# Performance work log

Hardware: AMD Instinct MI355X
Metric: run time of the kernel (lower is better)

Reference implementation:

```python
import jax, jax.numpy as jnp
import numpy as np
from math import sqrt

B, H, S, D = 4, 16, 2048, 64
NEG = -1000000000.0

def setup_inputs() -> dict:
    key = jax.random.key(0)
    kq, kk, kv, km = jax.random.split(key, 4)
    Q = jax.random.normal(kq, (B, H, S, D), dtype=jnp.float32)
    K = jax.random.normal(kk, (B, H, S, D), dtype=jnp.float32)
    V = jax.random.normal(kv, (B, H, S, D), dtype=jnp.float32)
    mask = jax.random.uniform(km, (B, 1, S, S)) < 0.1
    return {"Q": Q, "K": K, "V": V, "mask": mask}

def reference(Q, K, V, mask) -> jnp.ndarray:
    # scores: [B,H,S,S]
    scores = jnp.einsum('bhqd,bhkd->bhqk', Q, K)
    scores = jnp.where(mask, NEG, scores)
    attn = jax.nn.softmax(scores / sqrt(Q.shape[-1]), axis=-1)
    return jnp.einsum('bhqk,bhkd->bhqd', attn, V)
```

## Files before the change

kernel.cpp:

```cpp
#include <hip/hip_runtime.h>


#define SEQ 2048
#define DIM 64
#define NBH 64
#define LOG2E 1.44269504088896340736f
#define SCL (0.125f * LOG2E)
#define NEG_SCALED -1.25e8f

typedef short bf16x8 __attribute__((ext_vector_type(8)));
typedef float f32x4 __attribute__((ext_vector_type(4)));

static __device__ __forceinline__ unsigned short f2bf(float f) {
    unsigned int u = __float_as_uint(f);
    u += 0x7fffu + ((u >> 16) & 1u);
    return (unsigned short)(u >> 16);
}

#define GLD16(gp, lp) __builtin_amdgcn_global_load_lds( \
    (const __attribute__((address_space(1))) unsigned int*)(gp), \
    (__attribute__((address_space(3))) unsigned int*)(lp), 16, 0, 0)

__global__ __launch_bounds__(256)
void cvt_k_kernel(const float* __restrict__ K, unsigned short* __restrict__ Kb) {
    size_t i0 = ((size_t)blockIdx.x * 256 + threadIdx.x) * 8;
    float4 a = *(const float4*)(K + i0);
    float4 b = *(const float4*)(K + i0 + 4);
    union { uint4 u; unsigned short s[8]; } w;
    w.s[0] = f2bf(a.x); w.s[1] = f2bf(a.y); w.s[2] = f2bf(a.z); w.s[3] = f2bf(a.w);
    w.s[4] = f2bf(b.x); w.s[5] = f2bf(b.y); w.s[6] = f2bf(b.z); w.s[7] = f2bf(b.w);
    *(uint4*)(Kb + i0) = w.u;
}

__global__ __launch_bounds__(256)
void cvt_vt_kernel(const float* __restrict__ V, unsigned short* __restrict__ Vt) {
    __shared__ __align__(16) unsigned short T[64 * 64];
    const int bh = blockIdx.y;
    const int k0 = blockIdx.x * 64;
    const int t  = threadIdx.x;

    {
        const int kk = t >> 2;
        const int c  = t & 3;
        const int cs = c ^ ((kk >> 3) & 3);
        const float* vp = V + ((size_t)bh * SEQ + k0 + kk) * DIM + c * 16;
        union { uint4 u[2]; unsigned short s[16]; } w;
        #pragma unroll
        for (int j = 0; j < 16; ++j) w.s[j] = f2bf(vp[j]);
        *(uint4*)&T[kk * 64 + cs * 16]     = w.u[0];
        *(uint4*)&T[kk * 64 + cs * 16 + 8] = w.u[1];
    }
    __syncthreads();

    {
        const int kc = t & 7;
        const int dp = t >> 3;
        const int ch = (dp >> 3) ^ (kc & 3);
        const unsigned int* T32 = (const unsigned int*)T;
        union { uint4 u; unsigned short s[8]; } o0, o1;
        #pragma unroll
        for (int i = 0; i < 8; ++i) {
            unsigned int v = T32[(8 * kc + i) * 32 + ch * 8 + (dp & 7)];
            o0.s[i] = (unsigned short)v;
            o1.s[i] = (unsigned short)(v >> 16);
        }
        unsigned short* op = Vt + ((size_t)bh * DIM + 2 * dp) * SEQ + k0 + 8 * kc;
        *(uint4*)op         = o0.u;
        *(uint4*)(op + SEQ) = o1.u;
    }
}

__global__ __launch_bounds__(256)
void pack_mask_kernel(const int* __restrict__ M, unsigned int* __restrict__ Mp) {
    size_t w = (size_t)blockIdx.x * 256 + threadIdx.x;
    const int4* p = (const int4*)(M + w * 32);
    unsigned int m = 0;
    #pragma unroll
    for (int j = 0; j < 8; ++j) {
        int4 v = p[j];
        m |= (unsigned int)(v.x != 0) << (4 * j);
        m |= (unsigned int)(v.y != 0) << (4 * j + 1);
        m |= (unsigned int)(v.z != 0) << (4 * j + 2);
        m |= (unsigned int)(v.w != 0) << (4 * j + 3);
    }
    Mp[w] = m;
}

__global__ __launch_bounds__(256, 4)
void attn_main_kernel(const float* __restrict__ Q,
                      const unsigned short* __restrict__ Kb,
                      const unsigned short* __restrict__ Vt,
                      const unsigned int* __restrict__ Mp,
                      float* __restrict__ O)
{
    const int bh   = blockIdx.y;
    const int b    = bh >> 4;
    const int q0   = blockIdx.x * 128;
    const int tid  = threadIdx.x;
    const int wave = tid >> 6;
    const int lane = tid & 63;
    const int quad = lane >> 4;
    const int l16  = lane & 15;

    __shared__ __align__(16) unsigned short Kt[2][32 * 64];
    __shared__ __align__(16) unsigned short Vs[2][64 * 32];
    __shared__ __align__(16) unsigned short P[4][32][36];

    const unsigned short* Kbh = Kb + (size_t)bh * SEQ * DIM;
    const unsigned short* Vbh = Vt + (size_t)bh * SEQ * DIM;

    bf16x8 qf[2][2];
    {
        const float* Qb = Q + (size_t)bh * SEQ * DIM;
        #pragma unroll
        for (int qh = 0; qh < 2; ++qh) {
            const float* qp = Qb + (size_t)(q0 + wave * 32 + qh * 16 + l16) * DIM + quad * 8;
            #pragma unroll
            for (int dc = 0; dc < 2; ++dc) {
                float4 x = *(const float4*)(qp + dc * 32);
                float4 y = *(const float4*)(qp + dc * 32 + 4);
                qf[qh][dc][0] = (short)f2bf(x.x * SCL); qf[qh][dc][1] = (short)f2bf(x.y * SCL);
                qf[qh][dc][2] = (short)f2bf(x.z * SCL); qf[qh][dc][3] = (short)f2bf(x.w * SCL);
                qf[qh][dc][4] = (short)f2bf(y.x * SCL); qf[qh][dc][5] = (short)f2bf(y.y * SCL);
                qf[qh][dc][6] = (short)f2bf(y.z * SCL); qf[qh][dc][7] = (short)f2bf(y.w * SCL);
            }
        }
    }

    const int kkey  = wave * 8 + (lane >> 3);
    const int kclog = (lane & 7) ^ (lane >> 3);
    const unsigned short* kg = Kbh + (size_t)kkey * DIM + kclog * 8;
    const int vd    = wave * 16 + (lane >> 2);
    const int vclog = (lane & 3) ^ ((lane >> 2) & 3);
    const unsigned short* vg = Vbh + (size_t)vd * SEQ + vclog * 8;
    unsigned short* kl[2] = { &Kt[0][wave * 512], &Kt[1][wave * 512] };
    unsigned short* vl[2] = { &Vs[0][wave * 512], &Vs[1][wave * 512] };

    const unsigned int* mrow = Mp + ((size_t)b * SEQ + q0 + wave * 32) * (SEQ / 32);

    f32x4 acc[2][4];
    #pragma unroll
    for (int qh = 0; qh < 2; ++qh)
        #pragma unroll
        for (int dg = 0; dg < 4; ++dg) acc[qh][dg] = (f32x4){0.f, 0.f, 0.f, 0.f};
    float lsum[2][4] = {{0.f,0.f,0.f,0.f},{0.f,0.f,0.f,0.f}};

    GLD16(kg, kl[0]);
    GLD16(vg, vl[0]);

    for (int it = 0; it < SEQ / 32; ++it) {
        __syncthreads();

        unsigned int mw[2][4];
        #pragma unroll
        for (int qh = 0; qh < 2; ++qh)
            #pragma unroll
            for (int r = 0; r < 4; ++r)
                mw[qh][r] = mrow[(qh * 16 + quad * 4 + r) * (SEQ / 32) + it];

        if (it + 1 < SEQ / 32) {
            const unsigned short* kgn = kg + (size_t)(it + 1) * 32 * DIM;
            const unsigned short* vgn = vg + (size_t)(it + 1) * 32;
            int nb = (it + 1) & 1;
            GLD16(kgn, kl[nb]);
            GLD16(vgn, vl[nb]);
        }

        const unsigned short* Ktb = Kt[it & 1];
        const unsigned short* Vsb = Vs[it & 1];

        f32x4 sc[2][2];
        sc[0][0] = (f32x4){0.f,0.f,0.f,0.f}; sc[0][1] = (f32x4){0.f,0.f,0.f,0.f};
        sc[1][0] = (f32x4){0.f,0.f,0.f,0.f}; sc[1][1] = (f32x4){0.f,0.f,0.f,0.f};
        #pragma unroll
        for (int nt = 0; nt < 2; ++nt) {
            #pragma unroll
            for (int dc = 0; dc < 2; ++dc) {
                const int key = nt * 16 + l16;
                const int cst = (dc * 4 + quad) ^ (l16 & 7);
                bf16x8 kf = *(const bf16x8*)(Ktb + key * DIM + cst * 8);
                sc[0][nt] = __builtin_amdgcn_mfma_f32_16x16x32_bf16(qf[0][dc], kf, sc[0][nt], 0, 0, 0);
                sc[1][nt] = __builtin_amdgcn_mfma_f32_16x16x32_bf16(qf[1][dc], kf, sc[1][nt], 0, 0, 0);
            }
        }

        #pragma unroll
        for (int qh = 0; qh < 2; ++qh) {
            #pragma unroll
            for (int r = 0; r < 4; ++r) {
                unsigned int t = mw[qh][r] >> l16;
                float a0 = __builtin_amdgcn_exp2f(sc[qh][0][r]);
                float a1 = __builtin_amdgcn_exp2f(sc[qh][1][r]);
                a0 = (t & 1u) ? 0.f : a0;
                a1 = (t & 0x10000u) ? 0.f : a1;
                lsum[qh][r] += a0 + a1;
                unsigned int u0 = __float_as_uint(a0) + 0x8000u;
                unsigned int u1 = __float_as_uint(a1) + 0x8000u;
                unsigned int pk = __builtin_amdgcn_perm(u1, u0, 0x07060302u);
                const int row = qh * 16 + quad * 4 + r;
                P[wave][row][l16]      = (unsigned short)pk;
                P[wave][row][l16 + 16] = (unsigned short)(pk >> 16);
            }
        }

        bf16x8 pf0 = *(const bf16x8*)&P[wave][l16][quad * 8];
        bf16x8 pf1 = *(const bf16x8*)&P[wave][16 + l16][quad * 8];

        #pragma unroll
        for (int dg = 0; dg < 4; ++dg) {
            const int d   = dg * 16 + l16;
            const int cst = quad ^ (l16 & 3);
            bf16x8 vf = *(const bf16x8*)(Vsb + d * 32 + cst * 8);
            acc[0][dg] = __builtin_amdgcn_mfma_f32_16x16x32_bf16(pf0, vf, acc[0][dg], 0, 0, 0);
            acc[1][dg] = __builtin_amdgcn_mfma_f32_16x16x32_bf16(pf1, vf, acc[1][dg], 0, 0, 0);
        }
    }

    float* Ob = O + (size_t)bh * SEQ * DIM;
    #pragma unroll
    for (int qh = 0; qh < 2; ++qh) {
        #pragma unroll
        for (int r = 0; r < 4; ++r) {
            float l = lsum[qh][r];
            #pragma unroll
            for (int off = 1; off < 16; off <<= 1)
                l += __shfl_xor(l, off, 16);
            float inv = 1.f / l;
            const int row = q0 + wave * 32 + qh * 16 + quad * 4 + r;
            #pragma unroll
            for (int dg = 0; dg < 4; ++dg)
                Ob[(size_t)row * DIM + dg * 16 + l16] = acc[qh][dg][r] * inv;
        }
    }
}

__global__ __launch_bounds__(256)
void attn_fallback_kernel(const float* __restrict__ Q,
                          const float* __restrict__ K,
                          const float* __restrict__ V,
                          const int* __restrict__ mask,
                          float* __restrict__ O)
{
    const int bh   = blockIdx.y;
    const int b    = bh >> 4;
    const int q0   = blockIdx.x * 64;
    const int tid  = threadIdx.x;
    const int wave = tid >> 6;
    const int lane = tid & 63;
    const int quad = lane >> 4;
    const int l16  = lane & 15;

    __shared__ __align__(16) unsigned short Klds[32][72];
    __shared__ __align__(16) unsigned short VT[64][40];
    __shared__ __align__(16) unsigned short Plds[4][16][40];

    const float* Qb = Q + (size_t)bh * SEQ * DIM;
    const float* Kb = K + (size_t)bh * SEQ * DIM;
    const float* Vb = V + (size_t)bh * SEQ * DIM;
    const int*   Mb = mask + (size_t)b * SEQ * SEQ;

    const int qrow_frag = q0 + wave * 16 + l16;
    bf16x8 qf0, qf1;
    {
        const float* qp = Qb + (size_t)qrow_frag * DIM + quad * 8;
        #pragma unroll
        for (int i = 0; i < 8; ++i) {
            qf0[i] = (short)f2bf(qp[i]);
            qf1[i] = (short)f2bf(qp[32 + i]);
        }
    }

    f32x4 acc[4];
    #pragma unroll
    for (int dg = 0; dg < 4; ++dg) acc[dg] = (f32x4){0.f, 0.f, 0.f, 0.f};
    float mrowv[4] = {-INFINITY, -INFINITY, -INFINITY, -INFINITY};
    float lrow[4] = {0.f, 0.f, 0.f, 0.f};

    const int skey = tid >> 3;
    const int sd0  = (tid & 7) * 8;
    const int vkey = tid & 31;
    const int vd0  = (tid >> 5) * 8;
    const int qrow_m = q0 + wave * 16 + quad * 4;

    for (int kb = 0; kb < SEQ; kb += 32) {
        __syncthreads();
        {
            const float* kp = Kb + (size_t)(kb + skey) * DIM + sd0;
            union { uint4 u4; unsigned short s[8]; } kw;
            #pragma unroll
            for (int i = 0; i < 8; ++i) kw.s[i] = f2bf(kp[i]);
            *(uint4*)&Klds[skey][sd0] = kw.u4;
        }
        {
            const float* vp = Vb + (size_t)(kb + vkey) * DIM + vd0;
            #pragma unroll
            for (int i = 0; i < 8; ++i) VT[vd0 + i][vkey] = f2bf(vp[i]);
        }
        __syncthreads();

        f32x4 sc[2];
        sc[0] = (f32x4){0.f, 0.f, 0.f, 0.f};
        sc[1] = (f32x4){0.f, 0.f, 0.f, 0.f};
        #pragma unroll
        for (int nt = 0; nt < 2; ++nt) {
            bf16x8 kf0 = *(const bf16x8*)&Klds[nt * 16 + l16][quad * 8];
            bf16x8 kf1 = *(const bf16x8*)&Klds[nt * 16 + l16][32 + quad * 8];
            sc[nt] = __builtin_amdgcn_mfma_f32_16x16x32_bf16(qf0, kf0, sc[nt], 0, 0, 0);
            sc[nt] = __builtin_amdgcn_mfma_f32_16x16x32_bf16(qf1, kf1, sc[nt], 0, 0, 0);
        }

        float x[2][4];
        #pragma unroll
        for (int nt = 0; nt < 2; ++nt)
            #pragma unroll
            for (int r = 0; r < 4; ++r) {
                int mv = Mb[(size_t)(qrow_m + r) * SEQ + kb + nt * 16 + l16];
                x[nt][r] = mv ? NEG_SCALED : sc[nt][r] * 0.125f;
            }

        float p[2][4];
        #pragma unroll
        for (int r = 0; r < 4; ++r) {
            float rm = fmaxf(x[0][r], x[1][r]);
            #pragma unroll
            for (int off = 1; off < 16; off <<= 1)
                rm = fmaxf(rm, __shfl_xor(rm, off, 16));
            float mn = fmaxf(mrowv[r], rm);
            float alpha = exp2f((mrowv[r] - mn) * LOG2E);
            mrowv[r] = mn;
            float p0 = exp2f((x[0][r] - mn) * LOG2E);
            float p1 = exp2f((x[1][r] - mn) * LOG2E);
            p[0][r] = p0; p[1][r] = p1;
            float rs = p0 + p1;
            #pragma unroll
            for (int off = 1; off < 16; off <<= 1)
                rs += __shfl_xor(rs, off, 16);
            lrow[r] = lrow[r] * alpha + rs;
            #pragma unroll
            for (int dg = 0; dg < 4; ++dg)
                acc[dg][r] *= alpha;
        }

        #pragma unroll
        for (int nt = 0; nt < 2; ++nt)
            #pragma unroll
            for (int r = 0; r < 4; ++r)
                Plds[wave][quad * 4 + r][nt * 16 + l16] = f2bf(p[nt][r]);

        bf16x8 pf = *(const bf16x8*)&Plds[wave][l16][quad * 8];

        #pragma unroll
        for (int dg = 0; dg < 4; ++dg) {
            bf16x8 vf = *(const bf16x8*)&VT[dg * 16 + l16][quad * 8];
            acc[dg] = __builtin_amdgcn_mfma_f32_16x16x32_bf16(pf, vf, acc[dg], 0, 0, 0);
        }
    }

    float* Ob = O + (size_t)bh * SEQ * DIM;
    #pragma unroll
    for (int r = 0; r < 4; ++r) {
        float inv = 1.f / lrow[r];
        #pragma unroll
        for (int dg = 0; dg < 4; ++dg)
            Ob[(size_t)(qrow_m + r) * DIM + dg * 16 + l16] = acc[dg][r] * inv;
    }
}

extern "C" void kernel_launch(void* const* d_in, const int* in_sizes, int n_in,
                              void* d_out, int out_size, void* d_ws, size_t ws_size,
                              hipStream_t stream) {
    const float* Q = (const float*)d_in[0];
    const float* K = (const float*)d_in[1];
    const float* V = (const float*)d_in[2];
    const int* mask = (const int*)d_in[3];
    float*        O = (float*)d_out;

    const size_t szK = (size_t)NBH * SEQ * DIM * 2;
    const size_t szV = (size_t)NBH * SEQ * DIM * 2;
    const size_t szM = (size_t)4 * SEQ * (SEQ / 32) * 4;
    const size_t need = szK + szV + szM;

    if (ws_size >= need) {
        unsigned short* Kb = (unsigned short*)d_ws;
        unsigned short* Vt = (unsigned short*)((char*)d_ws + szK);
        unsigned int*   Mp = (unsigned int*)((char*)d_ws + szK + szV);

        cvt_k_kernel<<<dim3((NBH * SEQ * DIM) / (256 * 8)), 256, 0, stream>>>(K, Kb);
        cvt_vt_kernel<<<dim3(SEQ / 64, NBH), 256, 0, stream>>>(V, Vt);
        pack_mask_kernel<<<dim3((4 * SEQ * (SEQ / 32)) / 256), 256, 0, stream>>>(mask, Mp);
        attn_main_kernel<<<dim3(SEQ / 128, NBH), 256, 0, stream>>>(Q, Kb, Vt, Mp, O);
    } else {
        attn_fallback_kernel<<<dim3(SEQ / 64, NBH), 256, 0, stream>>>(Q, K, V, mask, O);
    }
}
```

Before: 302.7 us.

## Switch attention to 32x32 MFMA with register-only P exchange and fused prep kernel

Rewrites the main attention loop around 32x32x16 bf16 MFMA. S is computed as K·Q^T, so each lane owns one query row and the probabilities pass to the PV MFMA through a cross-half lane shuffle rather than a shared-memory round trip. The mask is packed in a transposed layout so each lane loads a single word per iteration. The three preprocessing kernels are merged into one launch to cut launch overhead. In exchange it raises register pressure with 16-wide accumulators and adds a loop unroll.

```diff
diff --git a/kernel.cpp b/kernel.cpp
--- a/kernel.cpp
+++ b/kernel.cpp
@@ -10,6 +10,7 @@
 
 typedef short bf16x8 __attribute__((ext_vector_type(8)));
 typedef float f32x4 __attribute__((ext_vector_type(4)));
+typedef float f32x16 __attribute__((ext_vector_type(16)));
 
 static __device__ __forceinline__ unsigned short f2bf(float f) {
     unsigned int u = __float_as_uint(f);
@@ -22,75 +23,78 @@
     (__attribute__((address_space(3))) unsigned int*)(lp), 16, 0, 0)
 
 __global__ __launch_bounds__(256)
-void cvt_k_kernel(const float* __restrict__ K, unsigned short* __restrict__ Kb) {
-    size_t i0 = ((size_t)blockIdx.x * 256 + threadIdx.x) * 8;
-    float4 a = *(const float4*)(K + i0);
-    float4 b = *(const float4*)(K + i0 + 4);
-    union { uint4 u; unsigned short s[8]; } w;
-    w.s[0] = f2bf(a.x); w.s[1] = f2bf(a.y); w.s[2] = f2bf(a.z); w.s[3] = f2bf(a.w);
-    w.s[4] = f2bf(b.x); w.s[5] = f2bf(b.y); w.s[6] = f2bf(b.z); w.s[7] = f2bf(b.w);
-    *(uint4*)(Kb + i0) = w.u;
-}
-
-__global__ __launch_bounds__(256)
-void cvt_vt_kernel(const float* __restrict__ V, unsigned short* __restrict__ Vt) {
-    __shared__ __align__(16) unsigned short T[64 * 64];
-    const int bh = blockIdx.y;
-    const int k0 = blockIdx.x * 64;
-    const int t  = threadIdx.x;
-
-    {
-        const int kk = t >> 2;
-        const int c  = t & 3;
-        const int cs = c ^ ((kk >> 3) & 3);
-        const float* vp = V + ((size_t)bh * SEQ + k0 + kk) * DIM + c * 16;
-        union { uint4 u[2]; unsigned short s[16]; } w;
-        #pragma unroll
-        for (int j = 0; j < 16; ++j) w.s[j] = f2bf(vp[j]);
-        *(uint4*)&T[kk * 64 + cs * 16]     = w.u[0];
-        *(uint4*)&T[kk * 64 + cs * 16 + 8] = w.u[1];
-    }
-    __syncthreads();
-
-    {
-        const int kc = t & 7;
-        const int dp = t >> 3;
-        const int ch = (dp >> 3) ^ (kc & 3);
-        const unsigned int* T32 = (const unsigned int*)T;
-        union { uint4 u; unsigned short s[8]; } o0, o1;
-        #pragma unroll
-        for (int i = 0; i < 8; ++i) {
-            unsigned int v = T32[(8 * kc + i) * 32 + ch * 8 + (dp & 7)];
-            o0.s[i] = (unsigned short)v;
-            o1.s[i] = (unsigned short)(v >> 16);
-        }
-        unsigned short* op = Vt + ((size_t)bh * DIM + 2 * dp) * SEQ + k0 + 8 * kc;
-        *(uint4*)op         = o0.u;
-        *(uint4*)(op + SEQ) = o1.u;
-    }
-}
-
-__global__ __launch_bounds__(256)
-void pack_mask_kernel(const int* __restrict__ M, unsigned int* __restrict__ Mp) {
-    size_t w = (size_t)blockIdx.x * 256 + threadIdx.x;
-    const int4* p = (const int4*)(M + w * 32);
-    unsigned int m = 0;
-    #pragma unroll
-    for (int j = 0; j < 8; ++j) {
-        int4 v = p[j];
-        m |= (unsigned int)(v.x != 0) << (4 * j);
-        m |= (unsigned int)(v.y != 0) << (4 * j + 1);
-        m |= (unsigned int)(v.z != 0) << (4 * j + 2);
-        m |= (unsigned int)(v.w != 0) << (4 * j + 3);
-    }
-    Mp[w] = m;
+void prep_all_kernel(const float* __restrict__ K, const float* __restrict__ V,
+                     const int* __restrict__ M,
+                     unsigned short* __restrict__ Kb, unsigned short* __restrict__ Vt,
+                     unsigned int* __restrict__ Mpt) {
+    const int x = blockIdx.x;
+    const int t = threadIdx.x;
+    if (x < 4096) {
+        size_t i0 = ((size_t)x * 256 + t) * 8;
+        float4 a = *(const float4*)(K + i0);
+        float4 b = *(const float4*)(K + i0 + 4);
+        union { uint4 u; unsigned short s[8]; } w;
+        w.s[0] = f2bf(a.x); w.s[1] = f2bf(a.y); w.s[2] = f2bf(a.z); w.s[3] = f2bf(a.w);
+        w.s[4] = f2bf(b.x); w.s[5] = f2bf(b.y); w.s[6] = f2bf(b.z); w.s[7] = f2bf(b.w);
+        *(uint4*)(Kb + i0) = w.u;
+    } else if (x < 6144) {
+        __shared__ __align__(16) unsigned short T[64 * 64];
+        const int vb = x - 4096;
+        const int bh = vb >> 5;
+        const int k0 = (vb & 31) * 64;
+        {
+            const int kk = t >> 2;
+            const int c  = t & 3;
+            const int cs = c ^ ((kk >> 3) & 3);
+            const float* vp = V + ((size_t)bh * SEQ + k0 + kk) * DIM + c * 16;
+            union { uint4 u[2]; unsigned short s[16]; } w;
+            #pragma unroll
+            for (int j = 0; j < 16; ++j) w.s[j] = f2bf(vp[j]);
+            *(uint4*)&T[kk * 64 + cs * 16]     = w.u[0];
+            *(uint4*)&T[kk * 64 + cs * 16 + 8] = w.u[1];
+        }
+        __syncthreads();
+        {
+            const int kc = t & 7;
+            const int dp = t >> 3;
+            const int ch = (dp >> 3) ^ (kc & 3);
+            const unsigned int* T32 = (const unsigned int*)T;
+            union { uint4 u; unsigned short s[8]; } o0, o1;
+            #pragma unroll
+            for (int i = 0; i < 8; ++i) {
+                unsigned int v = T32[(8 * kc + i) * 32 + ch * 8 + (dp & 7)];
+                o0.s[i] = (unsigned short)v;
+                o1.s[i] = (unsigned short)(v >> 16);
+            }
+            unsigned short* op = Vt + ((size_t)bh * DIM + 2 * dp) * SEQ + k0 + 8 * kc;
+            *(uint4*)op         = o0.u;
+            *(uint4*)(op + SEQ) = o1.u;
+        }
+    } else {
+        const int g = (x - 6144) * 256 + t;
+        const int b = g >> 17;
+        const int r = g & 131071;
+        const int q = r >> 6;
+        const int it = r & 63;
+        const int4* p = (const int4*)(M + (((size_t)b * SEQ + q) * SEQ + it * 32));
+        unsigned int m = 0;
+        #pragma unroll
+        for (int j = 0; j < 8; ++j) {
+            int4 v = p[j];
+            m |= (unsigned int)(v.x != 0) << (4 * j);
+            m |= (unsigned int)(v.y != 0) << (4 * j + 1);
+            m |= (unsigned int)(v.z != 0) << (4 * j + 2);
+            m |= (unsigned int)(v.w != 0) << (4 * j + 3);
+        }
+        Mpt[((size_t)b * 64 + it) * SEQ + q] = m;
+    }
 }
 
 __global__ __launch_bounds__(256, 4)
 void attn_main_kernel(const float* __restrict__ Q,
                       const unsigned short* __restrict__ Kb,
                       const unsigned short* __restrict__ Vt,
-                      const unsigned int* __restrict__ Mp,
+                      const unsigned int* __restrict__ Mpt,
                       float* __restrict__ O)
 {
     const int bh   = blockIdx.y;
@@ -99,31 +103,26 @@
     const int tid  = threadIdx.x;
     const int wave = tid >> 6;
     const int lane = tid & 63;
-    const int quad = lane >> 4;
-    const int l16  = lane & 15;
+    const int h    = lane >> 5;
+    const int q32  = lane & 31;
 
     __shared__ __align__(16) unsigned short Kt[2][32 * 64];
     __shared__ __align__(16) unsigned short Vs[2][64 * 32];
-    __shared__ __align__(16) unsigned short P[4][32][36];
 
     const unsigned short* Kbh = Kb + (size_t)bh * SEQ * DIM;
     const unsigned short* Vbh = Vt + (size_t)bh * SEQ * DIM;
 
-    bf16x8 qf[2][2];
+    bf16x8 qf[4];
     {
-        const float* Qb = Q + (size_t)bh * SEQ * DIM;
-        #pragma unroll
-        for (int qh = 0; qh < 2; ++qh) {
-            const float* qp = Qb + (size_t)(q0 + wave * 32 + qh * 16 + l16) * DIM + quad * 8;
-            #pragma unroll
-            for (int dc = 0; dc < 2; ++dc) {
-                float4 x = *(const float4*)(qp + dc * 32);
-                float4 y = *(const float4*)(qp + dc * 32 + 4);
-                qf[qh][dc][0] = (short)f2bf(x.x * SCL); qf[qh][dc][1] = (short)f2bf(x.y * SCL);
-                qf[qh][dc][2] = (short)f2bf(x.z * SCL); qf[qh][dc][3] = (short)f2bf(x.w * SCL);
-                qf[qh][dc][4] = (short)f2bf(y.x * SCL); qf[qh][dc][5] = (short)f2bf(y.y * SCL);
-                qf[qh][dc][6] = (short)f2bf(y.z * SCL); qf[qh][dc][7] = (short)f2bf(y.w * SCL);
-            }
+        const float* qp = Q + ((size_t)bh * SEQ + q0 + wave * 32 + q32) * DIM + h * 8;
+        #pragma unroll
+        for (int dc = 0; dc < 4; ++dc) {
+            float4 xx = *(const float4*)(qp + dc * 16);
+            float4 yy = *(const float4*)(qp + dc * 16 + 4);
+            qf[dc][0] = (short)f2bf(xx.x * SCL); qf[dc][1] = (short)f2bf(xx.y * SCL);
+            qf[dc][2] = (short)f2bf(xx.z * SCL); qf[dc][3] = (short)f2bf(xx.w * SCL);
+            qf[dc][4] = (short)f2bf(yy.x * SCL); qf[dc][5] = (short)f2bf(yy.y * SCL);
+            qf[dc][6] = (short)f2bf(yy.z * SCL); qf[dc][7] = (short)f2bf(yy.w * SCL);
         }
     }
 
@@ -136,27 +135,21 @@
     unsigned short* kl[2] = { &Kt[0][wave * 512], &Kt[1][wave * 512] };
     unsigned short* vl[2] = { &Vs[0][wave * 512], &Vs[1][wave * 512] };
 
-    const unsigned int* mrow = Mp + ((size_t)b * SEQ + q0 + wave * 32) * (SEQ / 32);
-
-    f32x4 acc[2][4];
+    const unsigned int* mp = Mpt + (size_t)b * 64 * SEQ + (q0 + wave * 32 + q32);
+
+    f32x16 acc[2];
     #pragma unroll
-    for (int qh = 0; qh < 2; ++qh)
-        #pragma unroll
-        for (int dg = 0; dg < 4; ++dg) acc[qh][dg] = (f32x4){0.f, 0.f, 0.f, 0.f};
-    float lsum[2][4] = {{0.f,0.f,0.f,0.f},{0.f,0.f,0.f,0.f}};
+    for (int i = 0; i < 16; ++i) { acc[0][i] = 0.f; acc[1][i] = 0.f; }
+    float lsum = 0.f;
 
     GLD16(kg, kl[0]);
     GLD16(vg, vl[0]);
 
+    #pragma unroll 2
     for (int it = 0; it < SEQ / 32; ++it) {
         __syncthreads();
 
-        unsigned int mw[2][4];
-        #pragma unroll
-        for (int qh = 0; qh < 2; ++qh)
-            #pragma unroll
-            for (int r = 0; r < 4; ++r)
-                mw[qh][r] = mrow[(qh * 16 + quad * 4 + r) * (SEQ / 32) + it];
+        unsigned int mw = mp[it * SEQ];
 
         if (it + 1 < SEQ / 32) {
             const unsigned short* kgn = kg + (size_t)(it + 1) * 32 * DIM;
@@ -169,67 +162,68 @@
         const unsigned short* Ktb = Kt[it & 1];
         const unsigned short* Vsb = Vs[it & 1];
 
-        f32x4 sc[2][2];
-        sc[0][0] = (f32x4){0.f,0.f,0.f,0.f}; sc[0][1] = (f32x4){0.f,0.f,0.f,0.f};
-        sc[1][0] = (f32x4){0.f,0.f,0.f,0.f}; sc[1][1] = (f32x4){0.f,0.f,0.f,0.f};
-        #pragma unroll
-        for (int nt = 0; nt < 2; ++nt) {
-            #pragma unroll
-            for (int dc = 0; dc < 2; ++dc) {
-                const int key = nt * 16 + l16;
-                const int cst = (dc * 4 + quad) ^ (l16 & 7);
-                bf16x8 kf = *(const bf16x8*)(Ktb + key * DIM + cst * 8);
-                sc[0][nt] = __builtin_amdgcn_mfma_f32_16x16x32_bf16(qf[0][dc], kf, sc[0][nt], 0, 0, 0);
-                sc[1][nt] = __builtin_amdgcn_mfma_f32_16x16x32_bf16(qf[1][dc], kf, sc[1][nt], 0, 0, 0);
+        f32x16 sc;
+        #pragma unroll
+        for (int i = 0; i < 16; ++i) sc[i] = 0.f;
+        #pragma unroll
+        for (int dc = 0; dc < 4; ++dc) {
+            const int pos = (dc * 2 + h) ^ (q32 & 7);
+            bf16x8 kf = *(const bf16x8*)(Ktb + q32 * 64 + pos * 8);
+            sc = __builtin_amdgcn_mfma_f32_32x32x16_bf16(kf, qf[dc], sc, 0, 0, 0);
+        }
+
+        const unsigned int mq = mw >> (4 * h);
+        float pv[16];
+        #pragma unroll
+        for (int r = 0; r < 16; ++r) {
+            const int s = (r & 3) + 8 * (r >> 2);
+            float e = __builtin_amdgcn_exp2f(sc[r]);
+            pv[r] = ((mq >> s) & 1u) ? 0.f : e;
+            lsum += pv[r];
+        }
+        unsigned int pk[8];
+        #pragma unroll
+        for (int m = 0; m < 8; ++m) {
+            unsigned int u0 = __float_as_uint(pv[2 * m])     + 0x8000u;
+            unsigned int u1 = __float_as_uint(pv[2 * m + 1]) + 0x8000u;
+            pk[m] = __builtin_amdgcn_perm(u1, u0, 0x07060302u);
+        }
+
+        #pragma unroll
+        for (int kk = 0; kk < 2; ++kk) {
+            unsigned int s0 = h ? pk[4 * kk + 0] : pk[4 * kk + 2];
+            unsigned int s1 = h ? pk[4 * kk + 1] : pk[4 * kk + 3];
+            unsigned int r0 = (unsigned int)__shfl_xor((int)s0, 32);
+            unsigned int r1 = (unsigned int)__shfl_xor((int)s1, 32);
+            union { unsigned int u[4]; bf16x8 v; } fr;
+            fr.u[0] = h ? r0 : pk[4 * kk + 0];
+            fr.u[1] = h ? r1 : pk[4 * kk + 1];
+            fr.u[2] = h ? pk[4 * kk + 2] : r0;
+            fr.u[3] = h ? pk[4 * kk + 3] : r1;
+
+            #pragma unroll
+            for (int dh = 0; dh < 2; ++dh) {
+                const int d   = dh * 32 + q32;
+                const int pos = (kk * 2 + h) ^ (d & 3);
+                bf16x8 vf = *(const bf16x8*)(Vsb + d * 32 + pos * 8);
+                acc[dh] = __builtin_amdgcn_mfma_f32_32x32x16_bf16(vf, fr.v, acc[dh], 0, 0, 0);
             }
         }
-
-        #pragma unroll
-        for (int qh = 0; qh < 2; ++qh) {
-            #pragma unroll
-            for (int r = 0; r < 4; ++r) {
-                unsigned int t = mw[qh][r] >> l16;
-                float a0 = __builtin_amdgcn_exp2f(sc[qh][0][r]);
-                float a1 = __builtin_amdgcn_exp2f(sc[qh][1][r]);
-                a0 = (t & 1u) ? 0.f : a0;
-                a1 = (t & 0x10000u) ? 0.f : a1;
-                lsum[qh][r] += a0 + a1;
-                unsigned int u0 = __float_as_uint(a0) + 0x8000u;
-                unsigned int u1 = __float_as_uint(a1) + 0x8000u;
-                unsigned int pk = __builtin_amdgcn_perm(u1, u0, 0x07060302u);
-                const int row = qh * 16 + quad * 4 + r;
-                P[wave][row][l16]      = (unsigned short)pk;
-                P[wave][row][l16 + 16] = (unsigned short)(pk >> 16);
-            }
-        }
-
-        bf16x8 pf0 = *(const bf16x8*)&P[wave][l16][quad * 8];
-        bf16x8 pf1 = *(const bf16x8*)&P[wave][16 + l16][quad * 8];
-
-        #pragma unroll
-        for (int dg = 0; dg < 4; ++dg) {
-            const int d   = dg * 16 + l16;
-            const int cst = quad ^ (l16 & 3);
-            bf16x8 vf = *(const bf16x8*)(Vsb + d * 32 + cst * 8);
-            acc[0][dg] = __builtin_amdgcn_mfma_f32_16x16x32_bf16(pf0, vf, acc[0][dg], 0, 0, 0);
-            acc[1][dg] = __builtin_amdgcn_mfma_f32_16x16x32_bf16(pf1, vf, acc[1][dg], 0, 0, 0);
-        }
-    }
-
-    float* Ob = O + (size_t)bh * SEQ * DIM;
+    }
+
+    lsum += __shfl_xor(lsum, 32);
+    const float inv = 1.f / lsum;
+    float* orow = O + ((size_t)bh * SEQ + q0 + wave * 32 + q32) * DIM;
     #pragma unroll
-    for (int qh = 0; qh < 2; ++qh) {
-        #pragma unroll
-        for (int r = 0; r < 4; ++r) {
-            float l = lsum[qh][r];
-            #pragma unroll
-            for (int off = 1; off < 16; off <<= 1)
-                l += __shfl_xor(l, off, 16);
-            float inv = 1.f / l;
-            const int row = q0 + wave * 32 + qh * 16 + quad * 4 + r;
-            #pragma unroll
-            for (int dg = 0; dg < 4; ++dg)
-                Ob[(size_t)row * DIM + dg * 16 + l16] = acc[qh][dg][r] * inv;
+    for (int dh = 0; dh < 2; ++dh) {
+        #pragma unroll
+        for (int r23 = 0; r23 < 4; ++r23) {
+            float4 w;
+            w.x = acc[dh][4 * r23 + 0] * inv;
+            w.y = acc[dh][4 * r23 + 1] * inv;
+            w.z = acc[dh][4 * r23 + 2] * inv;
+            w.w = acc[dh][4 * r23 + 3] * inv;
+            *(float4*)(orow + dh * 32 + r23 * 8 + h * 4) = w;
         }
     }
 }
@@ -298,15 +292,15 @@
         }
         __syncthreads();
 
-        f32x4 sc[2];
-        sc[0] = (f32x4){0.f, 0.f, 0.f, 0.f};
-        sc[1] = (f32x4){0.f, 0.f, 0.f, 0.f};
+        f32x4 scr[2];
+        scr[0] = (f32x4){0.f, 0.f, 0.f, 0.f};
+        scr[1] = (f32x4){0.f, 0.f, 0.f, 0.f};
         #pragma unroll
         for (int nt = 0; nt < 2; ++nt) {
             bf16x8 kf0 = *(const bf16x8*)&Klds[nt * 16 + l16][quad * 8];
             bf16x8 kf1 = *(const bf16x8*)&Klds[nt * 16 + l16][32 + quad * 8];
-            sc[nt] = __builtin_amdgcn_mfma_f32_16x16x32_bf16(qf0, kf0, sc[nt], 0, 0, 0);
-            sc[nt] = __builtin_amdgcn_mfma_f32_16x16x32_bf16(qf1, kf1, sc[nt], 0, 0, 0);
+            scr[nt] = __builtin_amdgcn_mfma_f32_16x16x32_bf16(qf0, kf0, scr[nt], 0, 0, 0);
+            scr[nt] = __builtin_amdgcn_mfma_f32_16x16x32_bf16(qf1, kf1, scr[nt], 0, 0, 0);
         }
 
         float x[2][4];
@@ -315,7 +309,7 @@
             #pragma unroll
             for (int r = 0; r < 4; ++r) {
                 int mv = Mb[(size_t)(qrow_m + r) * SEQ + kb + nt * 16 + l16];
-                x[nt][r] = mv ? NEG_SCALED : sc[nt][r] * 0.125f;
+                x[nt][r] = mv ? NEG_SCALED : scr[nt][r] * 0.125f;
             }
 
         float p[2][4];
@@ -383,12 +377,10 @@
     if (ws_size >= need) {
         unsigned short* Kb = (unsigned short*)d_ws;
         unsigned short* Vt = (unsigned short*)((char*)d_ws + szK);
-        unsigned int*   Mp = (unsigned int*)((char*)d_ws + szK + szV);
-
-        cvt_k_kernel<<<dim3((NBH * SEQ * DIM) / (256 * 8)), 256, 0, stream>>>(K, Kb);
-        cvt_vt_kernel<<<dim3(SEQ / 64, NBH), 256, 0, stream>>>(V, Vt);
-        pack_mask_kernel<<<dim3((4 * SEQ * (SEQ / 32)) / 256), 256, 0, stream>>>(mask, Mp);
-        attn_main_kernel<<<dim3(SEQ / 128, NBH), 256, 0, stream>>>(Q, Kb, Vt, Mp, O);
+        unsigned int*  Mpt = (unsigned int*)((char*)d_ws + szK + szV);
+
+        prep_all_kernel<<<dim3(8192), 256, 0, stream>>>(K, V, mask, Kb, Vt, Mpt);
+        attn_main_kernel<<<dim3(SEQ / 128, NBH), 256, 0, stream>>>(Q, Kb, Vt, Mpt, O);
     } else {
         attn_fallback_kernel<<<dim3(SEQ / 64, NBH), 256, 0, stream>>>(Q, K, V, mask, O);
     }
```

Result: faster. 290.7 us (-4.0%).
